# Optimization experiments

Measured on AMD Instinct MI355X. Metric: run time of the kernel, lower is better.

Reference implementation:

```python
import jax, jax.numpy as jnp
import numpy as np

IN_DIM = 256
K = 64
NB = 64  # num_blocks
N = NB * K
BATCH = 4096
DT = 0.05
TAU_EPS = 1e-6


def setup_inputs() -> dict:
    key = jax.random.key(0)
    ks = jax.random.split(key, 10)
    def xavier(k_, shape, fan_in, fan_out):
        lim = np.sqrt(6.0 / (fan_in + fan_out))
        return jax.random.uniform(k_, shape, jnp.float32, -lim, lim)
    return {
        "y": jax.random.normal(ks[0], (BATCH, N), jnp.float32),
        "u_t": jax.random.normal(ks[1], (BATCH, IN_DIM), jnp.float32),
        "tau_raw": jnp.zeros((N,), jnp.float32),
        "W_in_w": xavier(ks[2], (K, IN_DIM), IN_DIM, K),
        "W_in_b": jnp.zeros((K,), jnp.float32),
        "W_fwd_w": xavier(ks[3], (NB - 1, K, K), K, K),
        "W_fwd_b": jnp.zeros((NB - 1, K), jnp.float32),
        "W_rec_w": xavier(ks[4], (NB, K, K), K, K),
        "W_rec_b": jnp.zeros((NB, K), jnp.float32),
        "E_l": xavier(ks[5], (NB, K, K), K, K),
        "E_l_r": xavier(ks[6], (NB, K, K), K, K),
    }


def reference(y, u_t, tau_raw, W_in_w, W_in_b, W_fwd_w, W_fwd_b, W_rec_w, W_rec_b, E_l, E_l_r):
    yb = y.reshape(-1, NB, K)  # [batch, B, k]
    tau = jax.nn.softplus(tau_raw).reshape(NB, K) + TAU_EPS  # [B, k]
    # input drive for block 0 (torch Linear: x @ W^T + b)
    net0 = jnp.tanh(u_t @ W_in_w.T + W_in_b)  # [batch, k]
    # forward coupling for blocks 1..B-1, batched over blocks
    prev = yb[:, :-1, :]  # [batch, B-1, k]
    net_fwd = jnp.tanh(jnp.einsum('bji,joi->bjo', prev, W_fwd_w) + W_fwd_b)
    net_out = jnp.concatenate([net0[:, None, :], net_fwd], axis=1)  # [batch, B, k]
    # recurrent coupling, all blocks
    net_rec = jnp.tanh(jnp.einsum('bji,joi->bjo', yb, W_rec_w) + W_rec_b)
    decay = 1.0 / tau + jnp.abs(net_out) + jnp.abs(net_rec)  # [batch, B, k]
    drive = jnp.einsum('joi,bji->bjo', E_l, net_out) + jnp.einsum('joi,bji->bjo', E_l_r, net_rec)
    y_new = (yb + DT * drive) / (1.0 + DT * decay)
    return y_new.reshape(-1, N)
```

## Files before the change

kernel.cpp:

```cpp
#include <hip/hip_runtime.h>


#define IN_DIM 256
#define K 64
#define NB 64
#define BATCH 4096
#define NTOT 4096
#define DTC 0.05f
#define TAU_EPS 1e-6f
#define NSTR 72

#define WS_WREC 0
#define WS_EL   (64 * 4096)
#define WS_ELR  (128 * 4096)
#define WS_WFWD (192 * 4096)
#define WS_WIN  (255 * 4096)
#define WS_BLOCKS 259

typedef __bf16 bf16;
typedef bf16 bf16x8 __attribute__((ext_vector_type(8)));
typedef float f32x4 __attribute__((ext_vector_type(4)));

__device__ __forceinline__ float fast_tanh(float x) {
    float e = __expf(2.0f * x);
    return 1.0f - 2.0f * __builtin_amdgcn_rcpf(e + 1.0f);
}

__device__ __forceinline__ bf16x8 bfrag(const bf16* __restrict__ base,
                                        int kh, int ct, int lofs) {
    return *(const bf16x8*)(base + ((((kh * 4 + ct) << 6) + lofs) << 3));
}

__device__ __forceinline__ void load_afrag(const float* __restrict__ rowp,
                                           bf16x8& f0, bf16x8& f1) {
    float4 a0 = *(const float4*)(rowp);
    float4 a1 = *(const float4*)(rowp + 4);
    float4 a2 = *(const float4*)(rowp + 32);
    float4 a3 = *(const float4*)(rowp + 36);
    f0 = (bf16x8){ (bf16)a0.x, (bf16)a0.y, (bf16)a0.z, (bf16)a0.w,
                   (bf16)a1.x, (bf16)a1.y, (bf16)a1.z, (bf16)a1.w };
    f1 = (bf16x8){ (bf16)a2.x, (bf16)a2.y, (bf16)a2.z, (bf16)a2.w,
                   (bf16)a3.x, (bf16)a3.y, (bf16)a3.z, (bf16)a3.w };
}

__global__ __launch_bounds__(256)
void perm_weights(const float* __restrict__ W_in_w, const float* __restrict__ W_fwd_w,
                  const float* __restrict__ W_rec_w, const float* __restrict__ E_l,
                  const float* __restrict__ E_l_r, bf16* __restrict__ wsb) {
    const int g = blockIdx.x;
    const float* src;
    int stride;
    if (g < 64)       { src = W_rec_w + (size_t)g * 4096;         stride = 64;  }
    else if (g < 128) { src = E_l     + (size_t)(g - 64) * 4096;  stride = 64;  }
    else if (g < 192) { src = E_l_r   + (size_t)(g - 128) * 4096; stride = 64;  }
    else if (g < 255) { src = W_fwd_w + (size_t)(g - 192) * 4096; stride = 64;  }
    else              { src = W_in_w + (g - 255) * 64;            stride = 256; }
    bf16* dst = wsb + (size_t)g * 4096;
    const int tid = threadIdx.x;
#pragma unroll
    for (int h = 0; h < 2; ++h) {
        int c = tid * 2 + h;
        int kh = c >> 8, ct = (c >> 6) & 3, l16 = (c >> 2) & 15, quad = c & 3;
        const float* s = src + (ct * 16 + l16) * stride + kh * 32 + quad * 8;
        float4 a = *(const float4*)s;
        float4 b = *(const float4*)(s + 4);
        bf16x8 p = { (bf16)a.x, (bf16)a.y, (bf16)a.z, (bf16)a.w,
                     (bf16)b.x, (bf16)b.y, (bf16)b.z, (bf16)b.w };
        *(bf16x8*)(dst + (size_t)c * 8) = p;
    }
}

__global__ __launch_bounds__(256, 6)
void ltcn_main(const float* __restrict__ y, const float* __restrict__ u_t,
               const float* __restrict__ tau_raw,
               const float* __restrict__ W_in_b, const float* __restrict__ W_fwd_b,
               const float* __restrict__ W_rec_b,
               const bf16* __restrict__ wsb, float* __restrict__ out) {
    __shared__ bf16 sNO[64 * NSTR];
    __shared__ bf16 sNR[64 * NSTR];

    const int tid  = threadIdx.x;
    const int j    = blockIdx.y;
    const int b0   = blockIdx.x * 64;
    const int wave = tid >> 6;
    const int lane = tid & 63;
    const int quad = lane >> 4;
    const int l16  = lane & 15;
    const int am   = wave * 16 + l16;
    const int lofs = l16 * 4 + quad;

    float bfv[4], brv[4], itv[4];
#pragma unroll
    for (int ct = 0; ct < 4; ++ct) {
        int n = ct * 16 + l16;
        brv[ct] = W_rec_b[j * K + n];
        bfv[ct] = j ? W_fwd_b[(j - 1) * K + n] : W_in_b[n];
        float x = tau_raw[j * K + n];
        float sp = (x > 15.0f) ? x : log1pf(__expf(x));
        itv[ct] = 1.0f / (sp + TAU_EPS);
    }

    f32x4 accF[4] = {}, accR[4] = {};
    {
        bf16x8 yc0, yc1;
        load_afrag(y + (size_t)(b0 + am) * NTOT + j * K + quad * 8, yc0, yc1);
        const bf16* Wr = wsb + WS_WREC + (size_t)j * 4096;
#pragma unroll
        for (int ct = 0; ct < 4; ++ct) {
            accR[ct] = __builtin_amdgcn_mfma_f32_16x16x32_bf16(yc0, bfrag(Wr, 0, ct, lofs), accR[ct], 0, 0, 0);
            accR[ct] = __builtin_amdgcn_mfma_f32_16x16x32_bf16(yc1, bfrag(Wr, 1, ct, lofs), accR[ct], 0, 0, 0);
        }
    }
    if (j) {
        bf16x8 yp0, yp1;
        load_afrag(y + (size_t)(b0 + am) * NTOT + (j - 1) * K + quad * 8, yp0, yp1);
        const bf16* Wf = wsb + WS_WFWD + (size_t)(j - 1) * 4096;
#pragma unroll
        for (int ct = 0; ct < 4; ++ct) {
            accF[ct] = __builtin_amdgcn_mfma_f32_16x16x32_bf16(yp0, bfrag(Wf, 0, ct, lofs), accF[ct], 0, 0, 0);
            accF[ct] = __builtin_amdgcn_mfma_f32_16x16x32_bf16(yp1, bfrag(Wf, 1, ct, lofs), accF[ct], 0, 0, 0);
        }
    } else {
        for (int kc = 0; kc < 4; ++kc) {
            bf16x8 u0, u1;
            load_afrag(u_t + (size_t)(b0 + am) * IN_DIM + kc * 64 + quad * 8, u0, u1);
            const bf16* Wf = wsb + WS_WIN + (size_t)kc * 4096;
#pragma unroll
            for (int ct = 0; ct < 4; ++ct) {
                accF[ct] = __builtin_amdgcn_mfma_f32_16x16x32_bf16(u0, bfrag(Wf, 0, ct, lofs), accF[ct], 0, 0, 0);
                accF[ct] = __builtin_amdgcn_mfma_f32_16x16x32_bf16(u1, bfrag(Wf, 1, ct, lofs), accF[ct], 0, 0, 0);
            }
        }
    }

    float absum[4][4];
#pragma unroll
    for (int ct = 0; ct < 4; ++ct) {
#pragma unroll
        for (int r = 0; r < 4; ++r) {
            float no = fast_tanh(accF[ct][r] + bfv[ct]);
            float nr = fast_tanh(accR[ct][r] + brv[ct]);
            absum[ct][r] = fabsf(no) + fabsf(nr);
            int m = wave * 16 + quad * 4 + r;
            int n = ct * 16 + l16;
            sNO[m * NSTR + n] = (bf16)no;
            sNR[m * NSTR + n] = (bf16)nr;
        }
    }
    bf16x8 aO0 = *(const bf16x8*)(sNO + am * NSTR + quad * 8);
    bf16x8 aO1 = *(const bf16x8*)(sNO + am * NSTR + quad * 8 + 32);
    bf16x8 aR0 = *(const bf16x8*)(sNR + am * NSTR + quad * 8);
    bf16x8 aR1 = *(const bf16x8*)(sNR + am * NSTR + quad * 8 + 32);

    f32x4 accD[4] = {};
    const bf16* El  = wsb + WS_EL  + (size_t)j * 4096;
    const bf16* Elr = wsb + WS_ELR + (size_t)j * 4096;
#pragma unroll
    for (int ct = 0; ct < 4; ++ct) {
        accD[ct] = __builtin_amdgcn_mfma_f32_16x16x32_bf16(aO0, bfrag(El,  0, ct, lofs), accD[ct], 0, 0, 0);
        accD[ct] = __builtin_amdgcn_mfma_f32_16x16x32_bf16(aO1, bfrag(El,  1, ct, lofs), accD[ct], 0, 0, 0);
        accD[ct] = __builtin_amdgcn_mfma_f32_16x16x32_bf16(aR0, bfrag(Elr, 0, ct, lofs), accD[ct], 0, 0, 0);
        accD[ct] = __builtin_amdgcn_mfma_f32_16x16x32_bf16(aR1, bfrag(Elr, 1, ct, lofs), accD[ct], 0, 0, 0);
    }

#pragma unroll
    for (int ct = 0; ct < 4; ++ct) {
#pragma unroll
        for (int r = 0; r < 4; ++r) {
            size_t gi = (size_t)(b0 + wave * 16 + quad * 4 + r) * NTOT + j * K + ct * 16 + l16;
            float decay = itv[ct] + absum[ct][r];
            out[gi] = (y[gi] + DTC * accD[ct][r]) * __builtin_amdgcn_rcpf(1.0f + DTC * decay);
        }
    }
}

extern "C" void kernel_launch(void* const* d_in, const int* in_sizes, int n_in,
                              void* d_out, int out_size, void* d_ws, size_t ws_size,
                              hipStream_t stream) {
    const float* y       = (const float*)d_in[0];
    const float* u_t     = (const float*)d_in[1];
    const float* tau_raw = (const float*)d_in[2];
    const float* W_in_w  = (const float*)d_in[3];
    const float* W_in_b  = (const float*)d_in[4];
    const float* W_fwd_w = (const float*)d_in[5];
    const float* W_fwd_b = (const float*)d_in[6];
    const float* W_rec_w = (const float*)d_in[7];
    const float* W_rec_b = (const float*)d_in[8];
    const float* E_l     = (const float*)d_in[9];
    const float* E_l_r   = (const float*)d_in[10];
    float* out = (float*)d_out;
    bf16* wsb = (bf16*)d_ws;

    hipLaunchKernelGGL(perm_weights, dim3(WS_BLOCKS), dim3(256), 0, stream,
                       W_in_w, W_fwd_w, W_rec_w, E_l, E_l_r, wsb);
    hipLaunchKernelGGL(ltcn_main, dim3(BATCH / 64, NB), dim3(256), 0, stream,
                       y, u_t, tau_raw, W_in_b, W_fwd_b, W_rec_b, wsb, out);
}
```

Measured before the change: 192.6 us.

## Stage current y block in shared memory and batch-prefetch weight fragments

The block's own 64x64 slice of y is loaded once into shared memory with coalesced float4 loads. It is then reused both for the MFMA A-fragment and for the final update, instead of being read from global twice with a scattered epilogue access. All eight B-fragments for each weight matrix are loaded before their MFMAs to raise memory-level parallelism, and the denominator is precomputed. The launch-bounds occupancy hint drops from 6 to 4 waves to make room for the extra registers and LDS, which may reduce latency hiding.

Result: faster. 174.3 us (-9.5%).

```diff
diff --git a/kernel.cpp b/kernel.cpp
--- a/kernel.cpp
+++ b/kernel.cpp
@@ -9,6 +9,7 @@
 #define DTC 0.05f
 #define TAU_EPS 1e-6f
 #define NSTR 72
+#define YSTR 68
 
 #define WS_WREC 0
 #define WS_EL   (64 * 4096)
@@ -70,14 +71,15 @@
     }
 }
 
-__global__ __launch_bounds__(256, 6)
+__global__ __launch_bounds__(256, 4)
 void ltcn_main(const float* __restrict__ y, const float* __restrict__ u_t,
                const float* __restrict__ tau_raw,
                const float* __restrict__ W_in_b, const float* __restrict__ W_fwd_b,
                const float* __restrict__ W_rec_b,
                const bf16* __restrict__ wsb, float* __restrict__ out) {
-    __shared__ bf16 sNO[64 * NSTR];
-    __shared__ bf16 sNR[64 * NSTR];
+    __shared__ float sY [64 * YSTR];
+    __shared__ bf16  sNO[64 * NSTR];
+    __shared__ bf16  sNR[64 * NSTR];
 
     const int tid  = threadIdx.x;
     const int j    = blockIdx.y;
@@ -89,6 +91,16 @@
     const int am   = wave * 16 + l16;
     const int lofs = l16 * 4 + quad;
 
+    {
+        int r  = lane >> 2;
+        int cb = (lane & 3) * 16;
+        const float* ysrc = y + (size_t)(b0 + wave * 16 + r) * NTOT + j * K + cb;
+        float* ydst = sY + (wave * 16 + r) * YSTR + cb;
+#pragma unroll
+        for (int i = 0; i < 4; ++i)
+            *(float4*)(ydst + i * 4) = *(const float4*)(ysrc + i * 4);
+    }
+
     float bfv[4], brv[4], itv[4];
 #pragma unroll
     for (int ct = 0; ct < 4; ++ct) {
@@ -100,47 +112,67 @@
         itv[ct] = 1.0f / (sp + TAU_EPS);
     }
 
+    bf16x8 yc0, yc1;
+    {
+        const float* p = sY + am * YSTR + quad * 8;
+        float4 a0 = *(const float4*)(p);
+        float4 a1 = *(const float4*)(p + 4);
+        float4 a2 = *(const float4*)(p + 32);
+        float4 a3 = *(const float4*)(p + 36);
+        yc0 = (bf16x8){ (bf16)a0.x, (bf16)a0.y, (bf16)a0.z, (bf16)a0.w,
+                        (bf16)a1.x, (bf16)a1.y, (bf16)a1.z, (bf16)a1.w };
+        yc1 = (bf16x8){ (bf16)a2.x, (bf16)a2.y, (bf16)a2.z, (bf16)a2.w,
+                        (bf16)a3.x, (bf16)a3.y, (bf16)a3.z, (bf16)a3.w };
+    }
+
     f32x4 accF[4] = {}, accR[4] = {};
     {
-        bf16x8 yc0, yc1;
-        load_afrag(y + (size_t)(b0 + am) * NTOT + j * K + quad * 8, yc0, yc1);
         const bf16* Wr = wsb + WS_WREC + (size_t)j * 4096;
-#pragma unroll
-        for (int ct = 0; ct < 4; ++ct) {
-            accR[ct] = __builtin_amdgcn_mfma_f32_16x16x32_bf16(yc0, bfrag(Wr, 0, ct, lofs), accR[ct], 0, 0, 0);
-            accR[ct] = __builtin_amdgcn_mfma_f32_16x16x32_bf16(yc1, bfrag(Wr, 1, ct, lofs), accR[ct], 0, 0, 0);
+        bf16x8 wr[8];
+#pragma unroll
+        for (int t = 0; t < 8; ++t) wr[t] = bfrag(Wr, t >> 2, t & 3, lofs);
+#pragma unroll
+        for (int ct = 0; ct < 4; ++ct) {
+            accR[ct] = __builtin_amdgcn_mfma_f32_16x16x32_bf16(yc0, wr[ct],     accR[ct], 0, 0, 0);
+            accR[ct] = __builtin_amdgcn_mfma_f32_16x16x32_bf16(yc1, wr[4 + ct], accR[ct], 0, 0, 0);
         }
     }
     if (j) {
         bf16x8 yp0, yp1;
         load_afrag(y + (size_t)(b0 + am) * NTOT + (j - 1) * K + quad * 8, yp0, yp1);
         const bf16* Wf = wsb + WS_WFWD + (size_t)(j - 1) * 4096;
-#pragma unroll
-        for (int ct = 0; ct < 4; ++ct) {
-            accF[ct] = __builtin_amdgcn_mfma_f32_16x16x32_bf16(yp0, bfrag(Wf, 0, ct, lofs), accF[ct], 0, 0, 0);
-            accF[ct] = __builtin_amdgcn_mfma_f32_16x16x32_bf16(yp1, bfrag(Wf, 1, ct, lofs), accF[ct], 0, 0, 0);
+        bf16x8 wf[8];
+#pragma unroll
+        for (int t = 0; t < 8; ++t) wf[t] = bfrag(Wf, t >> 2, t & 3, lofs);
+#pragma unroll
+        for (int ct = 0; ct < 4; ++ct) {
+            accF[ct] = __builtin_amdgcn_mfma_f32_16x16x32_bf16(yp0, wf[ct],     accF[ct], 0, 0, 0);
+            accF[ct] = __builtin_amdgcn_mfma_f32_16x16x32_bf16(yp1, wf[4 + ct], accF[ct], 0, 0, 0);
         }
     } else {
         for (int kc = 0; kc < 4; ++kc) {
             bf16x8 u0, u1;
             load_afrag(u_t + (size_t)(b0 + am) * IN_DIM + kc * 64 + quad * 8, u0, u1);
             const bf16* Wf = wsb + WS_WIN + (size_t)kc * 4096;
+            bf16x8 wf[8];
+#pragma unroll
+            for (int t = 0; t < 8; ++t) wf[t] = bfrag(Wf, t >> 2, t & 3, lofs);
 #pragma unroll
             for (int ct = 0; ct < 4; ++ct) {
-                accF[ct] = __builtin_amdgcn_mfma_f32_16x16x32_bf16(u0, bfrag(Wf, 0, ct, lofs), accF[ct], 0, 0, 0);
-                accF[ct] = __builtin_amdgcn_mfma_f32_16x16x32_bf16(u1, bfrag(Wf, 1, ct, lofs), accF[ct], 0, 0, 0);
+                accF[ct] = __builtin_amdgcn_mfma_f32_16x16x32_bf16(u0, wf[ct],     accF[ct], 0, 0, 0);
+                accF[ct] = __builtin_amdgcn_mfma_f32_16x16x32_bf16(u1, wf[4 + ct], accF[ct], 0, 0, 0);
             }
         }
     }
 
-    float absum[4][4];
+    float den[4][4];
 #pragma unroll
     for (int ct = 0; ct < 4; ++ct) {
 #pragma unroll
         for (int r = 0; r < 4; ++r) {
             float no = fast_tanh(accF[ct][r] + bfv[ct]);
             float nr = fast_tanh(accR[ct][r] + brv[ct]);
-            absum[ct][r] = fabsf(no) + fabsf(nr);
+            den[ct][r] = 1.0f + DTC * (itv[ct] + fabsf(no) + fabsf(nr));
             int m = wave * 16 + quad * 4 + r;
             int n = ct * 16 + l16;
             sNO[m * NSTR + n] = (bf16)no;
@@ -153,23 +185,37 @@
     bf16x8 aR1 = *(const bf16x8*)(sNR + am * NSTR + quad * 8 + 32);
 
     f32x4 accD[4] = {};
-    const bf16* El  = wsb + WS_EL  + (size_t)j * 4096;
-    const bf16* Elr = wsb + WS_ELR + (size_t)j * 4096;
+    {
+        const bf16* El = wsb + WS_EL + (size_t)j * 4096;
+        bf16x8 el[8];
+#pragma unroll
+        for (int t = 0; t < 8; ++t) el[t] = bfrag(El, t >> 2, t & 3, lofs);
+#pragma unroll
+        for (int ct = 0; ct < 4; ++ct) {
+            accD[ct] = __builtin_amdgcn_mfma_f32_16x16x32_bf16(aO0, el[ct],     accD[ct], 0, 0, 0);
+            accD[ct] = __builtin_amdgcn_mfma_f32_16x16x32_bf16(aO1, el[4 + ct], accD[ct], 0, 0, 0);
+        }
+    }
+    {
+        const bf16* Elr = wsb + WS_ELR + (size_t)j * 4096;
+        bf16x8 er[8];
+#pragma unroll
+        for (int t = 0; t < 8; ++t) er[t] = bfrag(Elr, t >> 2, t & 3, lofs);
+#pragma unroll
+        for (int ct = 0; ct < 4; ++ct) {
+            accD[ct] = __builtin_amdgcn_mfma_f32_16x16x32_bf16(aR0, er[ct],     accD[ct], 0, 0, 0);
+            accD[ct] = __builtin_amdgcn_mfma_f32_16x16x32_bf16(aR1, er[4 + ct], accD[ct], 0, 0, 0);
+        }
+    }
+
 #pragma unroll
     for (int ct = 0; ct < 4; ++ct) {
-        accD[ct] = __builtin_amdgcn_mfma_f32_16x16x32_bf16(aO0, bfrag(El,  0, ct, lofs), accD[ct], 0, 0, 0);
-        accD[ct] = __builtin_amdgcn_mfma_f32_16x16x32_bf16(aO1, bfrag(El,  1, ct, lofs), accD[ct], 0, 0, 0);
-        accD[ct] = __builtin_amdgcn_mfma_f32_16x16x32_bf16(aR0, bfrag(Elr, 0, ct, lofs), accD[ct], 0, 0, 0);
-        accD[ct] = __builtin_amdgcn_mfma_f32_16x16x32_bf16(aR1, bfrag(Elr, 1, ct, lofs), accD[ct], 0, 0, 0);
-    }
-
-#pragma unroll
-    for (int ct = 0; ct < 4; ++ct) {
 #pragma unroll
         for (int r = 0; r < 4; ++r) {
-            size_t gi = (size_t)(b0 + wave * 16 + quad * 4 + r) * NTOT + j * K + ct * 16 + l16;
-            float decay = itv[ct] + absum[ct][r];
-            out[gi] = (y[gi] + DTC * accD[ct][r]) * __builtin_amdgcn_rcpf(1.0f + DTC * decay);
+            int m = wave * 16 + quad * 4 + r;
+            float yv = sY[m * YSTR + ct * 16 + l16];
+            size_t gi = (size_t)(b0 + m) * NTOT + j * K + ct * 16 + l16;
+            out[gi] = (yv + DTC * accD[ct][r]) * __builtin_amdgcn_rcpf(den[ct][r]);
         }
     }
 }
```
